# Kernel tuning notes

Hardware: AMD Instinct MI355X
Metric: run time of the kernel (lower is better)

## Reference

```python
import jax, jax.numpy as jnp
import numpy as np

# Fixed architecture constants from the source
B, T, D, V, L, H = 4096, 128, 64, 65, 3, 8
HD = D // H  # head_size = 8
DF = 4 * D   # 256


def _layernorm(x, g, b, eps=1e-5):
    mu = jnp.mean(x, axis=-1, keepdims=True)
    var = jnp.mean(jnp.square(x - mu), axis=-1, keepdims=True)
    return (x - mu) * jax.lax.rsqrt(var + eps) * g + b


def setup_inputs() -> dict:
    key = jax.random.key(0)
    ks = iter(jax.random.split(key, 64))
    s = 0.02
    n = lambda shape: jax.random.normal(next(ks), shape, dtype=jnp.float32) * s
    inp = {
        "tok_emb": n((V, D)),
        "pos_emb": n((T, D)),
        # per-block params stacked on leading layer dim L=3
        "ln1_g": jnp.ones((L, D), jnp.float32), "ln1_b": jnp.zeros((L, D), jnp.float32),
        "wq": n((L, D, D)), "wk": n((L, D, D)), "wv": n((L, D, D)),
        "wo": n((L, D, D)), "bo": jnp.zeros((L, D), jnp.float32),
        "ln2_g": jnp.ones((L, D), jnp.float32), "ln2_b": jnp.zeros((L, D), jnp.float32),
        "w1": n((L, D, DF)), "b1": jnp.zeros((L, DF), jnp.float32),
        "w2": n((L, DF, D)), "b2": jnp.zeros((L, D), jnp.float32),
        "lnf_g": jnp.ones((D,), jnp.float32), "lnf_b": jnp.zeros((D,), jnp.float32),
        "lm_w": n((D, V)), "lm_b": jnp.zeros((V,), jnp.float32),
        "idx": jax.random.randint(next(ks), (B, T), 0, V),
        "targets": jax.random.randint(next(ks), (B, T), 0, V),
    }
    return inp


def _forward(tok_emb, pos_emb, ln1_g, ln1_b, wq, wk, wv, wo, bo,
             ln2_g, ln2_b, w1, b1, w2, b2, lnf_g, lnf_b, lm_w, lm_b,
             idx, targets):
    b, t = idx.shape
    x = tok_emb[idx] + pos_emb[:t]  # [B,T,D]
    mask = jnp.tril(jnp.ones((t, t), bool))
    scale = 1.0 / np.sqrt(HD)
    for l in range(L):  # 3 structurally identical blocks (dropout = identity at eval)
        xn = _layernorm(x, ln1_g[l], ln1_b[l])
        # 8 per-head projections fused into one [D,D] matmul (concat along out dim)
        q = (xn @ wq[l]).reshape(b, t, H, HD)
        k = (xn @ wk[l]).reshape(b, t, H, HD)
        v = (xn @ wv[l]).reshape(b, t, H, HD)
        scores = jnp.einsum('bqhd,bkhd->bhqk', q, k) * scale
        scores = jnp.where(mask, scores, -jnp.inf)
        probs = jax.nn.softmax(scores, axis=-1)
        attn = jnp.einsum('bhqk,bkhd->bqhd', probs, v).reshape(b, t, D)
        x = x + attn @ wo[l] + bo[l]
        xn = _layernorm(x, ln2_g[l], ln2_b[l])
        x = x + jax.nn.relu(xn @ w1[l] + b1[l]) @ w2[l] + b2[l]
    x = _layernorm(x, lnf_g, lnf_b)
    logits = (x @ lm_w + lm_b).reshape(b * t, V)
    logp = jax.nn.log_softmax(logits, axis=-1)
    loss = -jnp.mean(jnp.take_along_axis(logp, targets.reshape(b * t, 1), axis=1))
    return logits, loss


def reference(tok_emb, pos_emb, ln1_g, ln1_b, wq, wk, wv, wo, bo,
              ln2_g, ln2_b, w1, b1, w2, b2, lnf_g, lnf_b, lm_w, lm_b,
              idx, targets):
    return _forward(tok_emb, pos_emb, ln1_g, ln1_b, wq, wk, wv, wo, bo,
                    ln2_g, ln2_b, w1, b1, w2, b2, lnf_g, lnf_b, lm_w, lm_b,
                    idx, targets)
```

## Files before the change

kernel.cpp:

```cpp
#include <hip/hip_runtime.h>
#include <hip/hip_bf16.h>

#define NB  4096
#define NT  128
#define ND  64
#define NV  65
#define NL  3
#define NH  8
#define NDF 256
#define NBT (NB*NT)

#define OFF_TOK   0
#define OFF_POS   4160
#define OFF_LN1G  12352
#define OFF_LN1B  12544
#define OFF_WQ    12736
#define OFF_WK    25024
#define OFF_WV    37312
#define OFF_WO    49600
#define OFF_BO    61888
#define OFF_LN2G  62080
#define OFF_LN2B  62272
#define OFF_W1    62464
#define OFF_B1    111616
// ... 152 lines not shown
    float var  = s2 * (1.f / 64.f) - mu * mu;
    float rstd = rsqrtf(var + 1e-5f);
    #pragma unroll
    for (int c = 0; c < 8; c++) {
        int cc = c0 + c;
        dst[r][cc] = (src[r][cc] - mu) * rstd * g[cc] + bb[cc];
    }
}

__device__ __forceinline__ void ln_frag_hi(const float (*src)[68],
        unsigned short* __restrict__ dhi,
        const float* __restrict__ g, const float* __restrict__ bb, int tid) {
    int r = tid >> 3, q = tid & 7, c0 = q * 8;
    float s = 0.f, s2 = 0.f;
    #pragma unroll
    for (int c = 0; c < 8; c++) { float v = src[r][c0 + c]; s += v; s2 += v * v; }
    s += __shfl_xor(s, 1);  s2 += __shfl_xor(s2, 1);
    s += __shfl_xor(s, 2);  s2 += __shfl_xor(s2, 2);
    s += __shfl_xor(s, 4);  s2 += __shfl_xor(s2, 4);
    float mu   = s  * (1.f / 64.f);
    float var  = s2 * (1.f / 64.f) - mu * mu;
    float rstd = rsqrtf(var + 1e-5f);
    unsigned uh[4];
    #pragma unroll
    for (int c2 = 0; c2 < 4; c2++) {
        float y0 = (src[r][c0 + c2*2    ] - mu) * rstd * g[c0 + c2*2    ] + bb[c0 + c2*2    ];
        float y1 = (src[r][c0 + c2*2 + 1] - mu) * rstd * g[c0 + c2*2 + 1] + bb[c0 + c2*2 + 1];
        uh[c2] = (unsigned)f2bf(y0) | ((unsigned)f2bf(y1) << 16);
    }
    int di = (((r >> 4) * 2 + (q >> 2)) * 64 + (q & 3) * 16 + (r & 15)) * 8;
    *(uint4*)(dhi + di) = make_uint4(uh[0], uh[1], uh[2], uh[3]);
}

__device__ __forceinline__ void fma16(const float* xr, const float* wr, float& a) {
    float4 x0 = *(const float4*)(xr);
    float4 x1 = *(const float4*)(xr + 4);
    float4 x2 = *(const float4*)(xr + 8);
    float4 x3 = *(const float4*)(xr + 12);
    a = fmaf(x0.x, wr[0],  a); a = fmaf(x0.y, wr[1],  a);
    a = fmaf(x0.z, wr[2],  a); a = fmaf(x0.w, wr[3],  a);
    a = fmaf(x1.x, wr[4],  a); a = fmaf(x1.y, wr[5],  a);
    a = fmaf(x1.z, wr[6],  a); a = fmaf(x1.w, wr[7],  a);
    a = fmaf(x2.x, wr[8],  a); a = fmaf(x2.y, wr[9],  a);
    a = fmaf(x2.z, wr[10], a); a = fmaf(x2.w, wr[11], a);
    a = fmaf(x3.x, wr[12], a); a = fmaf(x3.y, wr[13], a);
    a = fmaf(x3.z, wr[14], a); a = fmaf(x3.w, wr[15], a);
}

__device__ void ln_scalar(const float* x, float* o,
                          const float* g, const float* bb) {
    float mu = 0.f;
    for (int i = 0; i < ND; i++) mu += x[i];
    mu *= (1.f / 64.f);
    float var = 0.f;
    for (int i = 0; i < ND; i++) { float d = x[i] - mu; var += d * d; }
    var *= (1.f / 64.f);
    float rstd = rsqrtf(var + 1e-5f);
    for (int i = 0; i < ND; i++) o[i] = (x[i] - mu) * rstd * g[i] + bb[i];
}

__device__ __forceinline__ void store_o(unsigned short* xah, int mt, int head,
                                        int g, int cl, unsigned pk0, unsigned pk1) {
    if (cl < 8) {
        unsigned pk[2] = {pk0, pk1};
        #pragma unroll
        for (int i2 = 0; i2 < 4; i2++) {
            int r = mt * 16 + g * 4 + i2;
            int col = head * 8 + cl;
            unsigned v = pk[i2 >> 1];
            unsigned short hv = (unsigned short)((i2 & 1) ? (v >> 16) : (v & 0xffffu));
            int di = (((r >> 4) * 2 + (col >> 5)) * 64 + ((col >> 3) & 3) * 16
                      + (r & 15)) * 8 + (col & 7);
            xah[di] = hv;
        }
    }
}

__global__ __launch_bounds__(1024, 4) void gpt_fwd(
    const float* __restrict__ W, const unsigned short* __restrict__ pkw,
    int usepk, const void* __restrict__ idxp, const void* __restrict__ tgtp,
    float* __restrict__ out, float* __restrict__ loss_acc,
    const int* __restrict__ flags)
{
    __shared__ alignas(16) float xs[NT][68];
    __shared__ alignas(16) unsigned short xah[8192];
    __shared__ alignas(16) unsigned short uni[12288];
    __shared__ alignas(16) unsigned short zblk[8];
    __shared__ float wsum[8];

    unsigned short* q_l = uni;
    unsigned short* k_l = uni + 4096;
    unsigned short* vb  = uni + 8192;
    unsigned short* ha  = uni;

    const int tid  = threadIdx.x;
    const int lane = tid & 63;
    const int w    = tid >> 6;
    const int cl   = lane & 15;
    const int g    = lane >> 4;
    const int b    = blockIdx.x;
    const int fl   = *flags;
    if (!usepk || (fl & 8)) return;
    const bool i64 = !(fl & 4);
    const int*       idx32 = (const int*)idxp;
    const long long* idx64 = (const long long*)idxp;
    const int*       tgt32 = (const int*)tgtp;
    const long long* tgt64 = (const long long*)tgtp;

    if (tid < 8) zblk[tid] = 0;

    for (int e = tid * 4; e < NT * ND; e += 4096) {
        int r = e >> 6, c = e & 63;
        int n = b * NT + r;
        int tok = i64 ? (int)idx64[n] : idx32[n];
        float4 te = *(const float4*)&W[OFF_TOK + tok * ND + c];
        float4 pe = *(const float4*)&W[OFF_POS + r * ND + c];
        float4 xv;
        xv.x = te.x + pe.x; xv.y = te.y + pe.y;
        xv.z = te.z + pe.z; xv.w = te.w + pe.w;
        *(float4*)&xs[r][c] = xv;
    }
    __syncthreads();

    for (int lay = 0; lay < NL; lay++) {
        ln_frag_hi(xs, xah, W + OFF_LN1G + lay * 64, W + OFF_LN1B + lay * 64, tid);
        __syncthreads();

        unsigned ostash[2][2];
        const int headl = w & 3;

        #pragma unroll 1
        for (int hf = 0; hf < 2; hf++) {
            {
                const unsigned short* pbase = pkw + lay * 4096;
                #pragma unroll 1
                for (int i = 0; i < 3; i++) {
                    int ft = w * 3 + i;
                    int mat = ft >> 4;
                    int mt  = (ft >> 1) & 7;
                    int ntg = hf * 2 + (ft & 1);
                    const unsigned short* pb = pbase + mat * 12288 + ntg * 1024 + lane * 8;
                    f4v acc = {0.f, 0.f, 0.f, 0.f};
                    #pragma unroll
                    for (int kt = 0; kt < 2; kt++) {
                        s8v ah = *(const s8v*)(xah + ((mt * 2 + kt) * 64 + lane) * 8);
                        s8v bh = *(const s8v*)(pb + kt * 512);
                        s8v bl = *(const s8v*)(pb + PKLO + kt * 512);
                        acc = mfma16(ah, bh, acc);
                        acc = mfma16(ah, bl, acc);
                    }
                    int row0 = mt * 16 + g * 4;
                    int fullcol = ntg * 16 + cl;
                    int hl2 = (fullcol >> 3) & 3;
                    int dim = fullcol & 7;
                    if (mat == 0) {
                        #pragma unroll
                        for (int i2 = 0; i2 < 4; i2++)
                            q_l[(hl2 * 128 + row0 + i2) * 8 + dim] =
                                f2bf(acc[i2] * 0.35355339059327373f);
                    } else if (mat == 1) {
                        #pragma unroll
                        for (int i2 = 0; i2 < 4; i2++)
                            k_l[(hl2 * 128 + row0 + i2) * 8 + dim] = f2bf(acc[i2]);
                    } else {
                        #pragma unroll
                        for (int i2 = 0; i2 < 4; i2++) {
                            int key = row0 + i2;
                            vb[((hl2 * 4 + (key >> 5)) * 4 + ((key >> 3) & 3)) * 64
                               + dim * 8 + (key & 7)] = f2bf(acc[i2]);
                        }
                    }
                }
            }
            __syncthreads();

            {
                #pragma unroll 1
                for (int ti = 0; ti < 2; ti++) {
                    int mt = (w >> 2) + ti * 4;
                    const unsigned short* qsrc = (lane < 16)
                        ? q_l + (headl * 128 + mt * 16 + cl) * 8 : zblk;
                    s8v qb = *(const s8v*)qsrc;
                    float m = -1e30f, lsum = 0.f;
                    f4v o = {0.f, 0.f, 0.f, 0.f};
                    const int ktmax = mt >> 1;
                    #pragma unroll 1
                    for (int kt = 0; kt <= ktmax; kt++) {
                        f4v p0, p1;
                        {
                            const unsigned short* ksrc = (lane < 16)
                                ? k_l + (headl * 128 + (kt * 2) * 16 + cl) * 8 : zblk;
                            s8v kb = *(const s8v*)ksrc;
                            f4v s0 = {0.f, 0.f, 0.f, 0.f};
                            s0 = mfma16(kb, qb, s0);
                            if (kt * 2 == mt) {
                                #pragma unroll
                                for (int i2 = 0; i2 < 4; i2++)
                                    s0[i2] = (g * 4 + i2 <= cl) ? s0[i2] : -1e30f;
                            }
                            p0 = s0;
                        }
                        if (kt * 2 + 1 <= mt) {
                            const unsigned short* ksrc = (lane < 16)
                                ? k_l + (headl * 128 + (kt * 2 + 1) * 16 + cl) * 8 : zblk;
                            s8v kb = *(const s8v*)ksrc;
                            f4v s1 = {0.f, 0.f, 0.f, 0.f};
                            s1 = mfma16(kb, qb, s1);
                            if (kt * 2 + 1 == mt) {
                                #pragma unroll
                                for (int i2 = 0; i2 < 4; i2++)
                                    s1[i2] = (g * 4 + i2 <= cl) ? s1[i2] : -1e30f;
                            }
                            p1 = s1;
                        } else {
                            p1 = (f4v){-1e30f, -1e30f, -1e30f, -1e30f};
                        }
                        float bm = fmaxf(fmaxf(fmaxf(p0[0], p0[1]), fmaxf(p0[2], p0[3])),
                                         fmaxf(fmaxf(p1[0], p1[1]), fmaxf(p1[2], p1[3])));
                        bm = fmaxf(bm, __shfl_xor(bm, 16));
                        bm = fmaxf(bm, __shfl_xor(bm, 32));
                        float nm  = fmaxf(m, bm);
                        float fac = __expf(m - nm);
                        float ps = 0.f;
                        #pragma unroll
                        for (int i2 = 0; i2 < 4; i2++) {
                            p0[i2] = __expf(p0[i2] - nm); ps += p0[i2];
                            p1[i2] = __expf(p1[i2] - nm); ps += p1[i2];
                        }
                        ps += __shfl_xor(ps, 16);
                        ps += __shfl_xor(ps, 32);
                        lsum = lsum * fac + ps;
                        #pragma unroll
                        for (int i2 = 0; i2 < 4; i2++)
                            o[i2] *= __shfl(fac, g * 4 + i2);
                        float pe[8];
                        #pragma unroll
                        for (int e = 0; e < 8; e++) {
                            int src = ((g & 1) * 2 + (e >> 2)) * 16 + cl;
                            float a0 = __shfl(p0[e & 3], src);
                            float a1 = __shfl(p1[e & 3], src);
                            pe[e] = (g >> 1) ? a1 : a0;
                        }
                        union { unsigned u[4]; s8v v; } pu;
                        #pragma unroll
                        for (int j = 0; j < 4; j++)
                            pu.u[j] = (unsigned)f2bf(pe[2 * j]) |
                                      ((unsigned)f2bf(pe[2 * j + 1]) << 16);
                        s8v vf = *(const s8v*)(vb + ((headl * 4 + kt) * 4 + g) * 64
                                               + (cl & 7) * 8);
                        o = mfma16(pu.v, vf, o);
                        m = nm;
                    }
                    float inv = 1.f / lsum;
                    float invt[4];
                    #pragma unroll
                    for (int i2 = 0; i2 < 4; i2++) invt[i2] = __shfl(inv, g * 4 + i2);
                    unsigned pk0 = (unsigned)f2bf(o[0] * invt[0]) |
                                   ((unsigned)f2bf(o[1] * invt[1]) << 16);
                    unsigned pk1 = (unsigned)f2bf(o[2] * invt[2]) |
                                   ((unsigned)f2bf(o[3] * invt[3]) << 16);
                    if (hf == 0) {
                        ostash[ti][0] = pk0; ostash[ti][1] = pk1;
                    } else {
                        store_o(xah, mt, 4 + headl, g, cl, pk0, pk1);
                    }
                }
                if (hf == 1) {
                    #pragma unroll
                    for (int ti = 0; ti < 2; ti++) {
                        int mt = (w >> 2) + ti * 4;
                        store_o(xah, mt, headl, g, cl, ostash[ti][0], ostash[ti][1]);
                    }
                }
            }
            __syncthreads();
        }

        {
            const unsigned short* pbase = pkw + 36864 + lay * 4096;
            const float* bo = W + OFF_BO + lay * 64;
            #pragma unroll 1
            for (int i = 0; i < 2; i++) {
                int ft = w * 2 + i;
                int mt = ft >> 2, nt = ft & 3;
                const unsigned short* pb = pbase + nt * 1024 + lane * 8;
                f4v acc = {0.f, 0.f, 0.f, 0.f};
                #pragma unroll
                for (int kt = 0; kt < 2; kt++) {
                    s8v ah = *(const s8v*)(xah + ((mt * 2 + kt) * 64 + lane) * 8);
                    s8v bh = *(const s8v*)(pb + kt * 512);
                    s8v bl = *(const s8v*)(pb + PKLO + kt * 512);
                    acc = mfma16(ah, bh, acc);
                    acc = mfma16(ah, bl, acc);
                }
                int row0 = mt * 16 + g * 4, col = nt * 16 + cl;
                float bias = bo[col];
                #pragma unroll
                for (int i2 = 0; i2 < 4; i2++)
                    xs[row0 + i2][col] += acc[i2] + bias;
            }
        }
        __syncthreads();

        ln_frag_hi(xs, xah, W + OFF_LN2G + lay * 64, W + OFF_LN2B + lay * 64, tid);
        __syncthreads();

        #pragma unroll 1
        for (int ch = 0; ch < 4; ch++) {
            {
                const float* b1 = W + OFF_B1 + lay * 256;
                #pragma unroll 1
                for (int i = 0; i < 2; i++) {
                    int ft = w * 2 + i;
                    int mtl = ft >> 4, nt = ft & 15;
                    int mtg = ch * 2 + mtl;
                    const unsigned short* pb = pkw + 49152 + lay * 16384 + nt * 1024 + lane * 8;
                    f4v acc = {0.f, 0.f, 0.f, 0.f};
                    #pragma unroll
                    for (int kt = 0; kt < 2; kt++) {
                        s8v ah = *(const s8v*)(xah + ((mtg * 2 + kt) * 64 + lane) * 8);
                        s8v bh = *(const s8v*)(pb + kt * 512);
                        s8v bl = *(const s8v*)(pb + PKLO + kt * 512);
                        acc = mfma16(ah, bh, acc);
                        acc = mfma16(ah, bl, acc);
                    }
                    int col = nt * 16 + cl;
                    float bias = b1[col];
                    int kt2 = col >> 5, q2 = (col >> 3) & 3, e2 = col & 7;
                    #pragma unroll
                    for (int i2 = 0; i2 < 4; i2++) {
                        int lr = mtl * 16 + g * 4 + i2;
                        float hv = fmaxf(acc[i2] + bias, 0.f);
                        ha[((mtl * 8 + kt2) * 64 + q2 * 16 + (lr & 15)) * 8 + e2] = f2bf(hv);
                    }
                }
            }
            __syncthreads();
            {
                if (w < 8) {
                    const float* b2 = W + OFF_B2 + lay * 64;
                    int mtl = w >> 2, nt = w & 3;
                    const unsigned short* pb = pkw + 98304 + lay * 16384 + nt * 4096 + lane * 8;
                    f4v acc = {0.f, 0.f, 0.f, 0.f};
                    #pragma unroll 2
                    for (int kt = 0; kt < 8; kt++) {
                        s8v ah = *(const s8v*)(ha + ((mtl * 8 + kt) * 64 + lane) * 8);
                        s8v bh = *(const s8v*)(pb + kt * 512);
                        s8v bl = *(const s8v*)(pb + PKLO + kt * 512);
                        acc = mfma16(ah, bh, acc);
                        acc = mfma16(ah, bl, acc);
                    }
                    int row0 = ch * 32 + mtl * 16 + g * 4, col = nt * 16 + cl;
                    float bias = b2[col];
                    #pragma unroll
                    for (int i2 = 0; i2 < 4; i2++)
                        xs[row0 + i2][col] += acc[i2] + bias;
                }
            }
            __syncthreads();
        }
    }

    ln_frag_hi(xs, xah, W + OFF_LNFG, W + OFF_LNFB, tid);
    __syncthreads();

    if (w < 8) {
        int mt = w;
        const unsigned short* pb = pkw + 147456 + lane * 8;
        f4v acc[4];
        #pragma unroll
        for (int nt = 0; nt < 4; nt++) {
            f4v a = {0.f, 0.f, 0.f, 0.f};
            #pragma unroll
            for (int kt = 0; kt < 2; kt++) {
                s8v ah = *(const s8v*)(xah + ((mt * 2 + kt) * 64 + lane) * 8);
                s8v bh = *(const s8v*)(pb + nt * 1024 + kt * 512);
                s8v bl = *(const s8v*)(pb + PKLO + nt * 1024 + kt * 512);
                a = mfma16(ah, bh, a);
                a = mfma16(ah, bl, a);
            }
            float bias = W[OFF_LMB + nt * 16 + cl];
            #pragma unroll
            for (int i2 = 0; i2 < 4; i2++) a[i2] += bias;
            acc[nt] = a;
        }
        float l2 = 0.f;
        #pragma unroll
        for (int j = 0; j < 16; j++) {
            int d = g * 16 + j;
            int xi = ((mt * 2 + (d >> 5)) * 64 + ((d >> 3) & 3) * 16 + cl) * 8 + (d & 7);
            l2 += bf2f(xah[xi]) * W[OFF_LMW + d * 65 + 64];
        }
        l2 += __shfl_xor(l2, 16);
        l2 += __shfl_xor(l2, 32);
        l2 += W[OFF_LMB + 64];
        float l2t[4];
        #pragma unroll
        for (int i2 = 0; i2 < 4; i2++) l2t[i2] = __shfl(l2, g * 4 + i2);

        float wacc = 0.f;
        #pragma unroll
        for (int i2 = 0; i2 < 4; i2++) {
            float M = fmaxf(fmaxf(acc[0][i2], acc[1][i2]), fmaxf(acc[2][i2], acc[3][i2]));
            M = fmaxf(M, __shfl_xor(M, 1)); M = fmaxf(M, __shfl_xor(M, 2));
            M = fmaxf(M, __shfl_xor(M, 4)); M = fmaxf(M, __shfl_xor(M, 8));
            M = fmaxf(M, l2t[i2]);
            float ss = __expf(acc[0][i2] - M) + __expf(acc[1][i2] - M)
                     + __expf(acc[2][i2] - M) + __expf(acc[3][i2] - M);
            ss += __shfl_xor(ss, 1); ss += __shfl_xor(ss, 2);
            ss += __shfl_xor(ss, 4); ss += __shfl_xor(ss, 8);
            ss += __expf(l2t[i2] - M);
            float lse = M + logf(ss);
            int r = mt * 16 + g * 4 + i2;
            int row = b * NT + r;
            int tg = i64 ? (int)tgt64[row] : tgt32[row];
            float lt = 0.f;
            #pragma unroll
            for (int nt = 0; nt < 4; nt++)
                if (nt * 16 + cl == tg) lt += acc[nt][i2];
            wacc += lt;
            if (cl == 0) {
                if (tg == 64) wacc += l2t[i2];
                wacc -= lse;
                out[row * NV + 64] = l2t[i2];
            }
            #pragma unroll
            for (int nt = 0; nt < 4; nt++)
                out[row * NV + nt * 16 + cl] = acc[nt][i2];
        }
        wacc += __shfl_xor(wacc, 1);  wacc += __shfl_xor(wacc, 2);
        wacc += __shfl_xor(wacc, 4);  wacc += __shfl_xor(wacc, 8);
        wacc += __shfl_xor(wacc, 16); wacc += __shfl_xor(wacc, 32);
        if (lane == 0) wsum[w] = wacc;
    }
    __syncthreads();
    if (tid == 0) {
        float t = 0.f;
        #pragma unroll
        for (int wv = 0; wv < 8; wv++) t += wsum[wv];
        atomicAdd(loss_acc, t);
    }
    __syncthreads();

    if (b == 0 && tid == 0) {
        float x0[ND], xn0[ND], v0[ND], h0[NDF];
        int tok0 = i64 ? (int)idx64[0] : idx32[0];
        for (int c = 0; c < ND; c++)
            x0[c] = W[OFF_TOK + tok0 * ND + c] + W[OFF_POS + c];
        for (int l = 0; l < NL; l++) {
            ln_scalar(x0, xn0, W + OFF_LN1G + l * ND, W + OFF_LN1B + l * ND);
            for (int c = 0; c < ND; c++) {
                float a = 0.f;
                for (int i = 0; i < ND; i++)
                    a += xn0[i] * W[OFF_WV + l * ND * ND + i * ND + c];
                v0[c] = a;
            }
            for (int c = 0; c < ND; c++) {
                float a = W[OFF_BO + l * ND + c];
                for (int i = 0; i < ND; i++)
                    a += v0[i] * W[OFF_WO + l * ND * ND + i * ND + c];
                x0[c] += a;
            }
            ln_scalar(x0, xn0, W + OFF_LN2G + l * ND, W + OFF_LN2B + l * ND);
            for (int j = 0; j < NDF; j++) {
                float a = W[OFF_B1 + l * NDF + j];
                for (int i = 0; i < ND; i++)
                    a += xn0[i] * W[OFF_W1 + l * ND * NDF + i * NDF + j];
                h0[j] = fmaxf(a, 0.f);
            }
            for (int c = 0; c < ND; c++) {
                float a = W[OFF_B2 + l * ND + c];
                for (int j = 0; j < NDF; j++)
                    a += h0[j] * W[OFF_W2 + l * NDF * ND + j * ND + c];
                x0[c] += a;
            }
        }
        ln_scalar(x0, xn0, W + OFF_LNFG, W + OFF_LNFB);
        bool bad = false;
        for (int v = 0; v < NV; v++) {
            float lg = W[OFF_LMB + v];
            for (int i = 0; i < ND; i++)
                lg += xn0[i] * W[OFF_LMW + i * NV + v];
            if (!(fabsf(out[v] - lg) <= 0.1f)) bad = true;
        }
        if (bad) out[0] = 100.0f;
    }
}

__global__ __launch_bounds__(1024, 4) void gpt_fwd_valu(
    const float* __restrict__ W, int usepk,
    const void* __restrict__ idxp, const void* __restrict__ tgtp,
    float* __restrict__ out, float* __restrict__ loss_acc,
    const int* __restrict__ flags)
{
    const int fl = *flags;
    if (usepk && !(fl & 8)) return;

    __shared__ alignas(16) float xs[NT][68];
    __shared__ alignas(16) float xn[NT][68];
    __shared__ alignas(16) unsigned short qs[NT][72];
    __shared__ alignas(16) unsigned short ks[NT][72];
    __shared__ alignas(16) unsigned short vs[NT][72];
    __shared__ alignas(16) float hch[32][264];
    __shared__ float wsum[16];

    const int tid  = threadIdx.x;
    const int lane = tid & 63;
    const int w    = tid >> 6;
    const int b    = blockIdx.x;
    const bool i64 = !(fl & 4);
    const int*       idx32 = (const int*)idxp;
    const long long* idx64 = (const long long*)idxp;
    const int*       tgt32 = (const int*)tgtp;
    const long long* tgt64 = (const long long*)tgtp;

    for (int e = tid * 4; e < NT * ND; e += 4096) {
        int r = e >> 6, c = e & 63;
        int n = b * NT + r;
        int tok = i64 ? (int)idx64[n] : idx32[n];
        float4 te = *(const float4*)&W[OFF_TOK + tok * ND + c];
        float4 pe = *(const float4*)&W[OFF_POS + r * ND + c];
        float4 xv;
        xv.x = te.x + pe.x; xv.y = te.y + pe.y;
        xv.z = te.z + pe.z; xv.w = te.w + pe.w;
        *(float4*)&xs[r][c] = xv;
    }
    __syncthreads();
// ... 161 lines not shown
    __syncthreads();

    {
        const float* lmw = W + OFF_LMW;
        float wacc = 0.f;
        for (int rr = 0; rr < 8; rr++) {
            int r = w * 8 + rr;
            float lg  = W[OFF_LMB + lane];
            float lg2 = W[OFF_LMB + 64];
            #pragma unroll 8
            for (int i = 0; i < ND; i++) {
                float xv = xn[r][i];
                lg  = fmaf(xv, lmw[i * NV + lane], lg);
                lg2 = fmaf(xv, lmw[i * NV + 64],  lg2);
            }
            float M = lg;
            #pragma unroll
            for (int off = 32; off; off >>= 1) M = fmaxf(M, __shfl_xor(M, off));
            M = fmaxf(M, lg2);
            float ssum = __expf(lg - M);
            #pragma unroll
            for (int off = 32; off; off >>= 1) ssum += __shfl_xor(ssum, off);
            ssum += __expf(lg2 - M);
            float lse = M + logf(ssum);
            int row = b * NT + r;
            int tg  = i64 ? (int)tgt64[row] : tgt32[row];
            float lt = (tg < 64) ? __shfl(lg, tg) : lg2;
            wacc += lt - lse;
            out[row * NV + lane] = lg;
            if (lane == 0) out[row * NV + 64] = lg2;
        }
        if (lane == 0) wsum[w] = wacc;
        __syncthreads();
        if (tid == 0) {
            float t = 0.f;
            #pragma unroll
            for (int wv = 0; wv < 16; wv++) t += wsum[wv];
            atomicAdd(loss_acc, t);
        }
    }
}

__global__ void finalize_loss(const float* __restrict__ acc,
                              float* __restrict__ out) {
    out[NBT * NV] = -acc[0] * (1.f / (float)NBT);
}

extern "C" void kernel_launch(void* const* d_in, const int* in_sizes, int n_in,
                              void* d_out, int out_size, void* d_ws, size_t ws_size,
                              hipStream_t stream)
{
    static const int want[21] = {4160, 8192, 192, 192, 12288, 12288, 12288,
                                 12288, 192, 192, 192, 49152, 768, 49152, 192,
                                 64, 64, 4160, 65, 524288, 524288};
    int diag = 0;
    if (n_in != 21) diag = 3;
    else for (int i = 0; i < 21; i++) if (in_sizes[i] != want[i]) { diag = 3; break; }
    if (!diag && out_size != NBT * NV + 1) diag = 4;
    if (!diag && ws_size < (size_t)(OFF_FLAG + 1) * 4) diag = 5;
    if (diag) {
        diag_fill<<<(out_size + 255) / 256, 256, 0, stream>>>(
            (float*)d_out, out_size, (float)diag);
        return;
    }

    float* W = (float*)d_ws;
    float* loss_acc = W + OFF_LOSS;
    int*   flags    = (int*)(W + OFF_FLAG);
    hipMemsetAsync(W + OFF_LOSS, 0, 2 * sizeof(float), stream);

    detect_float<<<1, 256, 0, stream>>>((const unsigned short*)d_in[0], flags);
    detect_int  <<<1, 256, 0, stream>>>((const int*)d_in[19], flags);
    mfma_probe  <<<1, 64,  0, stream>>>(flags);

    CvtArgs a;
    for (int i = 0; i < 19; i++) a.p[i] = d_in[i];
    cvt_params<<<(CVT_TOTAL + 255) / 256, 256, 0, stream>>>(a, W, flags);

    int usepk = (ws_size >= NEED_WS) ? 1 : 0;
    unsigned short* pkw = (unsigned short*)(W + PKF);
    if (usepk)
        pack_weights<<<(PK_ELEMS + 255) / 256, 256, 0, stream>>>(W, pkw);

    gpt_fwd<<<NB, 1024, 0, stream>>>(W, pkw, usepk, d_in[19], d_in[20],
                                     (float*)d_out, loss_acc, flags);
    gpt_fwd_valu<<<NB, 1024, 0, stream>>>(W, usepk, d_in[19], d_in[20],
                                          (float*)d_out, loss_acc, flags);
    finalize_loss<<<1, 1, 0, stream>>>(loss_acc, (float*)d_out);
}
```

Measured before the change: 2.479 ms.

## Process two sequences per workgroup to reuse weight fragments across batches

Each 1024-thread workgroup now handles two batch sequences, with activation, fragment and scratch LDS buffers doubled. Weight fragments loaded from global memory are reused for both sequences' MFMAs, and the FFN2 and LM-head stages now use all 16 waves instead of 8. The grid is halved. This roughly doubles LDS per block, which may lower occupancy, and it raises register pressure because of the extra stash variables.

Measured after the change: 2.565 ms. 1.03x slower.

```diff
diff --git a/kernel.cpp b/kernel.cpp
--- a/kernel.cpp
+++ b/kernel.cpp
@@ -258,23 +258,18 @@
     float* __restrict__ out, float* __restrict__ loss_acc,
     const int* __restrict__ flags)
 {
-    __shared__ alignas(16) float xs[NT][68];
-    __shared__ alignas(16) unsigned short xah[8192];
-    __shared__ alignas(16) unsigned short uni[12288];
+    __shared__ alignas(16) float xs[2][NT][68];
+    __shared__ alignas(16) unsigned short xah[2][8192];
+    __shared__ alignas(16) unsigned short uni[2][12288];
     __shared__ alignas(16) unsigned short zblk[8];
-    __shared__ float wsum[8];
-
-    unsigned short* q_l = uni;
-    unsigned short* k_l = uni + 4096;
-    unsigned short* vb  = uni + 8192;
-    unsigned short* ha  = uni;
+    __shared__ float wsum[16];
 
     const int tid  = threadIdx.x;
     const int lane = tid & 63;
     const int w    = tid >> 6;
     const int cl   = lane & 15;
     const int g    = lane >> 4;
-    const int b    = blockIdx.x;
+    const int b0   = blockIdx.x * 2;
     const int fl   = *flags;
     if (!usepk || (fl & 8)) return;
     const bool i64 = !(fl & 4);
@@ -285,25 +280,29 @@
 
     if (tid < 8) zblk[tid] = 0;
 
-    for (int e = tid * 4; e < NT * ND; e += 4096) {
-        int r = e >> 6, c = e & 63;
-        int n = b * NT + r;
+    for (int e = tid * 4; e < 2 * NT * ND; e += 4096) {
+        int s = e >> 13;
+        int le = e & 8191;
+        int r = le >> 6, c = le & 63;
+        int n = (b0 + s) * NT + r;
         int tok = i64 ? (int)idx64[n] : idx32[n];
         float4 te = *(const float4*)&W[OFF_TOK + tok * ND + c];
         float4 pe = *(const float4*)&W[OFF_POS + r * ND + c];
         float4 xv;
         xv.x = te.x + pe.x; xv.y = te.y + pe.y;
         xv.z = te.z + pe.z; xv.w = te.w + pe.w;
-        *(float4*)&xs[r][c] = xv;
+        *(float4*)&xs[s][r][c] = xv;
     }
     __syncthreads();
 
     for (int lay = 0; lay < NL; lay++) {
-        ln_frag_hi(xs, xah, W + OFF_LN1G + lay * 64, W + OFF_LN1B + lay * 64, tid);
+        ln_frag_hi(xs[0], xah[0], W + OFF_LN1G + lay * 64, W + OFF_LN1B + lay * 64, tid);
+        ln_frag_hi(xs[1], xah[1], W + OFF_LN1G + lay * 64, W + OFF_LN1B + lay * 64, tid);
         __syncthreads();
 
-        unsigned ostash[2][2];
         const int headl = w & 3;
+        unsigned st0a = 0, st0b = 0, st1a = 0, st1b = 0;
+        unsigned st2a = 0, st2b = 0, st3a = 0, st3b = 0;
 
         #pragma unroll 1
         for (int hf = 0; hf < 2; hf++) {
@@ -316,34 +315,42 @@
                     int mt  = (ft >> 1) & 7;
                     int ntg = hf * 2 + (ft & 1);
                     const unsigned short* pb = pbase + mat * 12288 + ntg * 1024 + lane * 8;
-                    f4v acc = {0.f, 0.f, 0.f, 0.f};
-                    #pragma unroll
-                    for (int kt = 0; kt < 2; kt++) {
-                        s8v ah = *(const s8v*)(xah + ((mt * 2 + kt) * 64 + lane) * 8);
-                        s8v bh = *(const s8v*)(pb + kt * 512);
-                        s8v bl = *(const s8v*)(pb + PKLO + kt * 512);
-                        acc = mfma16(ah, bh, acc);
-                        acc = mfma16(ah, bl, acc);
-                    }
+                    s8v bh0 = *(const s8v*)(pb);
+                    s8v bl0 = *(const s8v*)(pb + PKLO);
+                    s8v bh1 = *(const s8v*)(pb + 512);
+                    s8v bl1 = *(const s8v*)(pb + PKLO + 512);
                     int row0 = mt * 16 + g * 4;
                     int fullcol = ntg * 16 + cl;
                     int hl2 = (fullcol >> 3) & 3;
                     int dim = fullcol & 7;
-                    if (mat == 0) {
-                        #pragma unroll
-                        for (int i2 = 0; i2 < 4; i2++)
-                            q_l[(hl2 * 128 + row0 + i2) * 8 + dim] =
-                                f2bf(acc[i2] * 0.35355339059327373f);
-                    } else if (mat == 1) {
-                        #pragma unroll
-                        for (int i2 = 0; i2 < 4; i2++)
-                            k_l[(hl2 * 128 + row0 + i2) * 8 + dim] = f2bf(acc[i2]);
-                    } else {
-                        #pragma unroll
-                        for (int i2 = 0; i2 < 4; i2++) {
-                            int key = row0 + i2;
-                            vb[((hl2 * 4 + (key >> 5)) * 4 + ((key >> 3) & 3)) * 64
-                               + dim * 8 + (key & 7)] = f2bf(acc[i2]);
+                    #pragma unroll
+                    for (int s = 0; s < 2; s++) {
+                        s8v a0 = *(const s8v*)(xah[s] + ((mt * 2    ) * 64 + lane) * 8);
+                        s8v a1 = *(const s8v*)(xah[s] + ((mt * 2 + 1) * 64 + lane) * 8);
+                        f4v acc = {0.f, 0.f, 0.f, 0.f};
+                        acc = mfma16(a0, bh0, acc);
+                        acc = mfma16(a0, bl0, acc);
+                        acc = mfma16(a1, bh1, acc);
+                        acc = mfma16(a1, bl1, acc);
+                        unsigned short* q_l = uni[s];
+                        unsigned short* k_l = uni[s] + 4096;
+                        unsigned short* vb  = uni[s] + 8192;
+                        if (mat == 0) {
+                            #pragma unroll
+                            for (int i2 = 0; i2 < 4; i2++)
+                                q_l[(hl2 * 128 + row0 + i2) * 8 + dim] =
+                                    f2bf(acc[i2] * 0.35355339059327373f);
+                        } else if (mat == 1) {
+                            #pragma unroll
+                            for (int i2 = 0; i2 < 4; i2++)
+                                k_l[(hl2 * 128 + row0 + i2) * 8 + dim] = f2bf(acc[i2]);
+                        } else {
+                            #pragma unroll
+                            for (int i2 = 0; i2 < 4; i2++) {
+                                int key = row0 + i2;
+                                vb[((hl2 * 4 + (key >> 5)) * 4 + ((key >> 3) & 3)) * 64
+                                   + dim * 8 + (key & 7)] = f2bf(acc[i2]);
+                            }
                         }
                     }
                 }
@@ -352,7 +359,11 @@
 
             {
                 #pragma unroll 1
-                for (int ti = 0; ti < 2; ti++) {
+                for (int sti = 0; sti < 4; sti++) {
+                    int s = sti & 1, ti = sti >> 1;
+                    unsigned short* q_l = uni[s];
+                    unsigned short* k_l = uni[s] + 4096;
+                    unsigned short* vb  = uni[s] + 8192;
                     int mt = (w >> 2) + ti * 4;
                     const unsigned short* qsrc = (lane < 16)
                         ? q_l + (headl * 128 + mt * 16 + cl) * 8 : zblk;
@@ -436,17 +447,22 @@
                     unsigned pk1 = (unsigned)f2bf(o[2] * invt[2]) |
                                    ((unsigned)f2bf(o[3] * invt[3]) << 16);
                     if (hf == 0) {
-                        ostash[ti][0] = pk0; ostash[ti][1] = pk1;
+                        switch (sti) {
+                            case 0:  st0a = pk0; st0b = pk1; break;
+                            case 1:  st1a = pk0; st1b = pk1; break;
+                            case 2:  st2a = pk0; st2b = pk1; break;
+                            default: st3a = pk0; st3b = pk1; break;
+                        }
                     } else {
-                        store_o(xah, mt, 4 + headl, g, cl, pk0, pk1);
+                        store_o(xah[s], mt, 4 + headl, g, cl, pk0, pk1);
                     }
                 }
                 if (hf == 1) {
-                    #pragma unroll
-                    for (int ti = 0; ti < 2; ti++) {
-                        int mt = (w >> 2) + ti * 4;
-                        store_o(xah, mt, headl, g, cl, ostash[ti][0], ostash[ti][1]);
-                    }
+                    int mt0 = (w >> 2), mt1 = (w >> 2) + 4;
+                    store_o(xah[0], mt0, headl, g, cl, st0a, st0b);
+                    store_o(xah[1], mt0, headl, g, cl, st1a, st1b);
+                    store_o(xah[0], mt1, headl, g, cl, st2a, st2b);
+                    store_o(xah[1], mt1, headl, g, cl, st3a, st3b);
                 }
             }
             __syncthreads();
@@ -460,88 +476,101 @@
                 int ft = w * 2 + i;
                 int mt = ft >> 2, nt = ft & 3;
                 const unsigned short* pb = pbase + nt * 1024 + lane * 8;
-                f4v acc = {0.f, 0.f, 0.f, 0.f};
-                #pragma unroll
-                for (int kt = 0; kt < 2; kt++) {
-                    s8v ah = *(const s8v*)(xah + ((mt * 2 + kt) * 64 + lane) * 8);
-                    s8v bh = *(const s8v*)(pb + kt * 512);
-                    s8v bl = *(const s8v*)(pb + PKLO + kt * 512);
-                    acc = mfma16(ah, bh, acc);
-                    acc = mfma16(ah, bl, acc);
-                }
+                s8v bh0 = *(const s8v*)(pb);
+                s8v bl0 = *(const s8v*)(pb + PKLO);
+                s8v bh1 = *(const s8v*)(pb + 512);
+                s8v bl1 = *(const s8v*)(pb + PKLO + 512);
                 int row0 = mt * 16 + g * 4, col = nt * 16 + cl;
                 float bias = bo[col];
                 #pragma unroll
-                for (int i2 = 0; i2 < 4; i2++)
-                    xs[row0 + i2][col] += acc[i2] + bias;
+                for (int s = 0; s < 2; s++) {
+                    s8v a0 = *(const s8v*)(xah[s] + ((mt * 2    ) * 64 + lane) * 8);
+                    s8v a1 = *(const s8v*)(xah[s] + ((mt * 2 + 1) * 64 + lane) * 8);
+                    f4v acc = {0.f, 0.f, 0.f, 0.f};
+                    acc = mfma16(a0, bh0, acc);
+                    acc = mfma16(a0, bl0, acc);
+                    acc = mfma16(a1, bh1, acc);
+                    acc = mfma16(a1, bl1, acc);
+                    #pragma unroll
+                    for (int i2 = 0; i2 < 4; i2++)
+                        xs[s][row0 + i2][col] += acc[i2] + bias;
+                }
             }
         }
         __syncthreads();
 
-        ln_frag_hi(xs, xah, W + OFF_LN2G + lay * 64, W + OFF_LN2B + lay * 64, tid);
+        ln_frag_hi(xs[0], xah[0], W + OFF_LN2G + lay * 64, W + OFF_LN2B + lay * 64, tid);
+        ln_frag_hi(xs[1], xah[1], W + OFF_LN2G + lay * 64, W + OFF_LN2B + lay * 64, tid);
         __syncthreads();
 
         #pragma unroll 1
         for (int ch = 0; ch < 4; ch++) {
             {
-                const float* b1 = W + OFF_B1 + lay * 256;
+                const float* b1p = W + OFF_B1 + lay * 256;
                 #pragma unroll 1
                 for (int i = 0; i < 2; i++) {
                     int ft = w * 2 + i;
                     int mtl = ft >> 4, nt = ft & 15;
                     int mtg = ch * 2 + mtl;
                     const unsigned short* pb = pkw + 49152 + lay * 16384 + nt * 1024 + lane * 8;
-                    f4v acc = {0.f, 0.f, 0.f, 0.f};
-                    #pragma unroll
-                    for (int kt = 0; kt < 2; kt++) {
-                        s8v ah = *(const s8v*)(xah + ((mtg * 2 + kt) * 64 + lane) * 8);
-                        s8v bh = *(const s8v*)(pb + kt * 512);
-                        s8v bl = *(const s8v*)(pb + PKLO + kt * 512);
-                        acc = mfma16(ah, bh, acc);
-                        acc = mfma16(ah, bl, acc);
-                    }
+                    s8v bh0 = *(const s8v*)(pb);
+                    s8v bl0 = *(const s8v*)(pb + PKLO);
+                    s8v bh1 = *(const s8v*)(pb + 512);
+                    s8v bl1 = *(const s8v*)(pb + PKLO + 512);
                     int col = nt * 16 + cl;
-                    float bias = b1[col];
+                    float bias = b1p[col];
                     int kt2 = col >> 5, q2 = (col >> 3) & 3, e2 = col & 7;
                     #pragma unroll
-                    for (int i2 = 0; i2 < 4; i2++) {
-                        int lr = mtl * 16 + g * 4 + i2;
-                        float hv = fmaxf(acc[i2] + bias, 0.f);
-                        ha[((mtl * 8 + kt2) * 64 + q2 * 16 + (lr & 15)) * 8 + e2] = f2bf(hv);
+                    for (int s = 0; s < 2; s++) {
+                        s8v a0 = *(const s8v*)(xah[s] + ((mtg * 2    ) * 64 + lane) * 8);
+                        s8v a1 = *(const s8v*)(xah[s] + ((mtg * 2 + 1) * 64 + lane) * 8);
+                        f4v acc = {0.f, 0.f, 0.f, 0.f};
+                        acc = mfma16(a0, bh0, acc);
+                        acc = mfma16(a0, bl0, acc);
+                        acc = mfma16(a1, bh1, acc);
+                        acc = mfma16(a1, bl1, acc);
+                        unsigned short* ha = uni[s];
+                        #pragma unroll
+                        for (int i2 = 0; i2 < 4; i2++) {
+                            int lr = mtl * 16 + g * 4 + i2;
+                            float hv = fmaxf(acc[i2] + bias, 0.f);
+                            ha[((mtl * 8 + kt2) * 64 + q2 * 16 + (lr & 15)) * 8 + e2] = f2bf(hv);
+                        }
                     }
                 }
             }
             __syncthreads();
             {
-                if (w < 8) {
-                    const float* b2 = W + OFF_B2 + lay * 64;
-                    int mtl = w >> 2, nt = w & 3;
-                    const unsigned short* pb = pkw + 98304 + lay * 16384 + nt * 4096 + lane * 8;
-                    f4v acc = {0.f, 0.f, 0.f, 0.f};
-                    #pragma unroll 2
-                    for (int kt = 0; kt < 8; kt++) {
-                        s8v ah = *(const s8v*)(ha + ((mtl * 8 + kt) * 64 + lane) * 8);
-                        s8v bh = *(const s8v*)(pb + kt * 512);
-                        s8v bl = *(const s8v*)(pb + PKLO + kt * 512);
-                        acc = mfma16(ah, bh, acc);
-                        acc = mfma16(ah, bl, acc);
-                    }
-                    int row0 = ch * 32 + mtl * 16 + g * 4, col = nt * 16 + cl;
-                    float bias = b2[col];
-                    #pragma unroll
-                    for (int i2 = 0; i2 < 4; i2++)
-                        xs[row0 + i2][col] += acc[i2] + bias;
-                }
+                const float* b2p = W + OFF_B2 + lay * 64;
+                int s = w >> 3, t8 = w & 7;
+                int mtl = t8 >> 2, nt = t8 & 3;
+                const unsigned short* pb = pkw + 98304 + lay * 16384 + nt * 4096 + lane * 8;
+                unsigned short* ha = uni[s];
+                f4v acc = {0.f, 0.f, 0.f, 0.f};
+                #pragma unroll 2
+                for (int kt = 0; kt < 8; kt++) {
+                    s8v ah = *(const s8v*)(ha + ((mtl * 8 + kt) * 64 + lane) * 8);
+                    s8v bh = *(const s8v*)(pb + kt * 512);
+                    s8v bl = *(const s8v*)(pb + PKLO + kt * 512);
+                    acc = mfma16(ah, bh, acc);
+                    acc = mfma16(ah, bl, acc);
+                }
+                int row0 = ch * 32 + mtl * 16 + g * 4, col = nt * 16 + cl;
+                float bias = b2p[col];
+                #pragma unroll
+                for (int i2 = 0; i2 < 4; i2++)
+                    xs[s][row0 + i2][col] += acc[i2] + bias;
             }
             __syncthreads();
         }
     }
 
-    ln_frag_hi(xs, xah, W + OFF_LNFG, W + OFF_LNFB, tid);
+    ln_frag_hi(xs[0], xah[0], W + OFF_LNFG, W + OFF_LNFB, tid);
+    ln_frag_hi(xs[1], xah[1], W + OFF_LNFG, W + OFF_LNFB, tid);
     __syncthreads();
 
-    if (w < 8) {
-        int mt = w;
+    {
+        int s = w >> 3, mt = w & 7;
         const unsigned short* pb = pkw + 147456 + lane * 8;
         f4v acc[4];
         #pragma unroll
@@ -549,7 +578,7 @@
             f4v a = {0.f, 0.f, 0.f, 0.f};
             #pragma unroll
             for (int kt = 0; kt < 2; kt++) {
-                s8v ah = *(const s8v*)(xah + ((mt * 2 + kt) * 64 + lane) * 8);
+                s8v ah = *(const s8v*)(xah[s] + ((mt * 2 + kt) * 64 + lane) * 8);
                 s8v bh = *(const s8v*)(pb + nt * 1024 + kt * 512);
                 s8v bl = *(const s8v*)(pb + PKLO + nt * 1024 + kt * 512);
                 a = mfma16(ah, bh, a);
@@ -565,7 +594,7 @@
         for (int j = 0; j < 16; j++) {
             int d = g * 16 + j;
             int xi = ((mt * 2 + (d >> 5)) * 64 + ((d >> 3) & 3) * 16 + cl) * 8 + (d & 7);
-            l2 += bf2f(xah[xi]) * W[OFF_LMW + d * 65 + 64];
+            l2 += bf2f(xah[s][xi]) * W[OFF_LMW + d * 65 + 64];
         }
         l2 += __shfl_xor(l2, 16);
         l2 += __shfl_xor(l2, 32);
@@ -588,7 +617,7 @@
             ss += __expf(l2t[i2] - M);
             float lse = M + logf(ss);
             int r = mt * 16 + g * 4 + i2;
-            int row = b * NT + r;
+            int row = (b0 + s) * NT + r;
             int tg = i64 ? (int)tgt64[row] : tgt32[row];
             float lt = 0.f;
             #pragma unroll
@@ -613,12 +642,12 @@
     if (tid == 0) {
         float t = 0.f;
         #pragma unroll
-        for (int wv = 0; wv < 8; wv++) t += wsum[wv];
+        for (int wv = 0; wv < 16; wv++) t += wsum[wv];
         atomicAdd(loss_acc, t);
     }
     __syncthreads();
 
-    if (b == 0 && tid == 0) {
+    if (b0 == 0 && tid == 0) {
         float x0[ND], xn0[ND], v0[ND], h0[NDF];
         int tok0 = i64 ? (int)idx64[0] : idx32[0];
         for (int c = 0; c < ND; c++)
@@ -946,8 +975,8 @@
     if (usepk)
         pack_weights<<<(PK_ELEMS + 255) / 256, 256, 0, stream>>>(W, pkw);
 
-    gpt_fwd<<<NB, 1024, 0, stream>>>(W, pkw, usepk, d_in[19], d_in[20],
-                                     (float*)d_out, loss_acc, flags);
+    gpt_fwd<<<NB / 2, 1024, 0, stream>>>(W, pkw, usepk, d_in[19], d_in[20],
+                                         (float*)d_out, loss_acc, flags);
     gpt_fwd_valu<<<NB, 1024, 0, stream>>>(W, usepk, d_in[19], d_in[20],
                                           (float*)d_out, loss_acc, flags);
     finalize_loss<<<1, 1, 0, stream>>>(loss_acc, (float*)d_out);
```

## Enlarge shared buffers to process all heads and full MLP in one pass

Applied to the files above, without the earlier changes.

Grows the shared scratch buffer from 24KB to 64KB so Q/K/V for all 8 heads and the full 128x256 hidden MLP activation fit at once. The QKV projection and attention become a single pass over all heads, and the MLP runs as one up-projection phase and one down-projection phase instead of four row chunks. This removes several block-wide barriers and idle waves (the w<8 branch in the down projection), and it makes the ostash register staging unnecessary. The cost is much higher LDS use per block, which may cut occupancy (launch bounds request 4 blocks of 1024 threads).

New measurement: 2.473 ms. Within noise of the previous version (-0.3%).

```diff
diff --git a/kernel.cpp b/kernel.cpp
--- a/kernel.cpp
+++ b/kernel.cpp
@@ -260,13 +260,13 @@
 {
     __shared__ alignas(16) float xs[NT][68];
     __shared__ alignas(16) unsigned short xah[8192];
-    __shared__ alignas(16) unsigned short uni[12288];
+    __shared__ alignas(16) unsigned short uni[32768];
     __shared__ alignas(16) unsigned short zblk[8];
     __shared__ float wsum[8];
 
     unsigned short* q_l = uni;
-    unsigned short* k_l = uni + 4096;
-    unsigned short* vb  = uni + 8192;
+    unsigned short* k_l = uni + 8192;
+    unsigned short* vb  = uni + 16384;
     unsigned short* ha  = uni;
 
     const int tid  = threadIdx.x;
@@ -302,155 +302,140 @@
         ln_frag_hi(xs, xah, W + OFF_LN1G + lay * 64, W + OFF_LN1B + lay * 64, tid);
         __syncthreads();
 
-        unsigned ostash[2][2];
-        const int headl = w & 3;
-
-        #pragma unroll 1
-        for (int hf = 0; hf < 2; hf++) {
-            {
-                const unsigned short* pbase = pkw + lay * 4096;
+        {
+            const unsigned short* pbase = pkw + lay * 4096;
+            #pragma unroll 1
+            for (int i = 0; i < 6; i++) {
+                int ft = w * 6 + i;
+                int mat = ft >> 5;
+                int rem = ft & 31;
+                int mt  = rem >> 2;
+                int ntg = rem & 3;
+                const unsigned short* pb = pbase + mat * 12288 + ntg * 1024 + lane * 8;
+                f4v acc = {0.f, 0.f, 0.f, 0.f};
+                #pragma unroll
+                for (int kt = 0; kt < 2; kt++) {
+                    s8v ah = *(const s8v*)(xah + ((mt * 2 + kt) * 64 + lane) * 8);
+                    s8v bh = *(const s8v*)(pb + kt * 512);
+                    s8v bl = *(const s8v*)(pb + PKLO + kt * 512);
+                    acc = mfma16(ah, bh, acc);
+                    acc = mfma16(ah, bl, acc);
+                }
+                int row0 = mt * 16 + g * 4;
+                int fullcol = ntg * 16 + cl;
+                int head = fullcol >> 3;
+                int dim  = fullcol & 7;
+                if (mat == 0) {
+                    #pragma unroll
+                    for (int i2 = 0; i2 < 4; i2++)
+                        q_l[(head * 128 + row0 + i2) * 8 + dim] =
+                            f2bf(acc[i2] * 0.35355339059327373f);
+                } else if (mat == 1) {
+                    #pragma unroll
+                    for (int i2 = 0; i2 < 4; i2++)
+                        k_l[(head * 128 + row0 + i2) * 8 + dim] = f2bf(acc[i2]);
+                } else {
+                    #pragma unroll
+                    for (int i2 = 0; i2 < 4; i2++) {
+                        int key = row0 + i2;
+                        vb[((head * 4 + (key >> 5)) * 4 + ((key >> 3) & 3)) * 64
+                           + dim * 8 + (key & 7)] = f2bf(acc[i2]);
+                    }
+                }
+            }
+        }
+        __syncthreads();
+
+        {
+            #pragma unroll 1
+            for (int ti = 0; ti < 4; ti++) {
+                int t = w + ti * 16;
+                int head = t & 7, mt = t >> 3;
+                const unsigned short* qsrc = (lane < 16)
+                    ? q_l + (head * 128 + mt * 16 + cl) * 8 : zblk;
+                s8v qb = *(const s8v*)qsrc;
+                float m = -1e30f, lsum = 0.f;
+                f4v o = {0.f, 0.f, 0.f, 0.f};
+                const int ktmax = mt >> 1;
                 #pragma unroll 1
-                for (int i = 0; i < 3; i++) {
-                    int ft = w * 3 + i;
-                    int mat = ft >> 4;
-                    int mt  = (ft >> 1) & 7;
-                    int ntg = hf * 2 + (ft & 1);
-                    const unsigned short* pb = pbase + mat * 12288 + ntg * 1024 + lane * 8;
-                    f4v acc = {0.f, 0.f, 0.f, 0.f};
-                    #pragma unroll
-                    for (int kt = 0; kt < 2; kt++) {
-                        s8v ah = *(const s8v*)(xah + ((mt * 2 + kt) * 64 + lane) * 8);
-                        s8v bh = *(const s8v*)(pb + kt * 512);
-                        s8v bl = *(const s8v*)(pb + PKLO + kt * 512);
-                        acc = mfma16(ah, bh, acc);
-                        acc = mfma16(ah, bl, acc);
+                for (int kt = 0; kt <= ktmax; kt++) {
+                    f4v p0, p1;
+                    {
+                        const unsigned short* ksrc = (lane < 16)
+                            ? k_l + (head * 128 + (kt * 2) * 16 + cl) * 8 : zblk;
+                        s8v kb = *(const s8v*)ksrc;
+                        f4v s0 = {0.f, 0.f, 0.f, 0.f};
+                        s0 = mfma16(kb, qb, s0);
+                        if (kt * 2 == mt) {
+                            #pragma unroll
+                            for (int i2 = 0; i2 < 4; i2++)
+                                s0[i2] = (g * 4 + i2 <= cl) ? s0[i2] : -1e30f;
+                        }
+                        p0 = s0;
                     }
-                    int row0 = mt * 16 + g * 4;
-                    int fullcol = ntg * 16 + cl;
-                    int hl2 = (fullcol >> 3) & 3;
-                    int dim = fullcol & 7;
-                    if (mat == 0) {
-                        #pragma unroll
-                        for (int i2 = 0; i2 < 4; i2++)
-                            q_l[(hl2 * 128 + row0 + i2) * 8 + dim] =
-                                f2bf(acc[i2] * 0.35355339059327373f);
-                    } else if (mat == 1) {
-                        #pragma unroll
-                        for (int i2 = 0; i2 < 4; i2++)
-                            k_l[(hl2 * 128 + row0 + i2) * 8 + dim] = f2bf(acc[i2]);
+                    if (kt * 2 + 1 <= mt) {
+                        const unsigned short* ksrc = (lane < 16)
+                            ? k_l + (head * 128 + (kt * 2 + 1) * 16 + cl) * 8 : zblk;
+                        s8v kb = *(const s8v*)ksrc;
+                        f4v s1 = {0.f, 0.f, 0.f, 0.f};
+                        s1 = mfma16(kb, qb, s1);
+                        if (kt * 2 + 1 == mt) {
+                            #pragma unroll
+                            for (int i2 = 0; i2 < 4; i2++)
+                                s1[i2] = (g * 4 + i2 <= cl) ? s1[i2] : -1e30f;
+                        }
+                        p1 = s1;
                     } else {
-                        #pragma unroll
-                        for (int i2 = 0; i2 < 4; i2++) {
-                            int key = row0 + i2;
-                            vb[((hl2 * 4 + (key >> 5)) * 4 + ((key >> 3) & 3)) * 64
-                               + dim * 8 + (key & 7)] = f2bf(acc[i2]);
-                        }
+                        p1 = (f4v){-1e30f, -1e30f, -1e30f, -1e30f};
                     }
-                }
-            }
-            __syncthreads();
-
-            {
-                #pragma unroll 1
-                for (int ti = 0; ti < 2; ti++) {
-                    int mt = (w >> 2) + ti * 4;
-                    const unsigned short* qsrc = (lane < 16)
-                        ? q_l + (headl * 128 + mt * 16 + cl) * 8 : zblk;
-                    s8v qb = *(const s8v*)qsrc;
-                    float m = -1e30f, lsum = 0.f;
-                    f4v o = {0.f, 0.f, 0.f, 0.f};
-                    const int ktmax = mt >> 1;
-                    #pragma unroll 1
-                    for (int kt = 0; kt <= ktmax; kt++) {
-                        f4v p0, p1;
-                        {
-                            const unsigned short* ksrc = (lane < 16)
-                                ? k_l + (headl * 128 + (kt * 2) * 16 + cl) * 8 : zblk;
-                            s8v kb = *(const s8v*)ksrc;
-                            f4v s0 = {0.f, 0.f, 0.f, 0.f};
-                            s0 = mfma16(kb, qb, s0);
-                            if (kt * 2 == mt) {
-                                #pragma unroll
-                                for (int i2 = 0; i2 < 4; i2++)
-                                    s0[i2] = (g * 4 + i2 <= cl) ? s0[i2] : -1e30f;
-                            }
-                            p0 = s0;
-                        }
-                        if (kt * 2 + 1 <= mt) {
-                            const unsigned short* ksrc = (lane < 16)
-                                ? k_l + (headl * 128 + (kt * 2 + 1) * 16 + cl) * 8 : zblk;
-                            s8v kb = *(const s8v*)ksrc;
-                            f4v s1 = {0.f, 0.f, 0.f, 0.f};
-                            s1 = mfma16(kb, qb, s1);
-                            if (kt * 2 + 1 == mt) {
-                                #pragma unroll
-                                for (int i2 = 0; i2 < 4; i2++)
-                                    s1[i2] = (g * 4 + i2 <= cl) ? s1[i2] : -1e30f;
-                            }
-                            p1 = s1;
-                        } else {
-                            p1 = (f4v){-1e30f, -1e30f, -1e30f, -1e30f};
-                        }
-                        float bm = fmaxf(fmaxf(fmaxf(p0[0], p0[1]), fmaxf(p0[2], p0[3])),
-                                         fmaxf(fmaxf(p1[0], p1[1]), fmaxf(p1[2], p1[3])));
-                        bm = fmaxf(bm, __shfl_xor(bm, 16));
-                        bm = fmaxf(bm, __shfl_xor(bm, 32));
-                        float nm  = fmaxf(m, bm);
-                        float fac = __expf(m - nm);
-                        float ps = 0.f;
-                        #pragma unroll
-                        for (int i2 = 0; i2 < 4; i2++) {
-                            p0[i2] = __expf(p0[i2] - nm); ps += p0[i2];
-                            p1[i2] = __expf(p1[i2] - nm); ps += p1[i2];
-                        }
-                        ps += __shfl_xor(ps, 16);
-                        ps += __shfl_xor(ps, 32);
-                        lsum = lsum * fac + ps;
-                        #pragma unroll
-                        for (int i2 = 0; i2 < 4; i2++)
-                            o[i2] *= __shfl(fac, g * 4 + i2);
-                        float pe[8];
-                        #pragma unroll
-                        for (int e = 0; e < 8; e++) {
-                            int src = ((g & 1) * 2 + (e >> 2)) * 16 + cl;
-                            float a0 = __shfl(p0[e & 3], src);
-                            float a1 = __shfl(p1[e & 3], src);
-                            pe[e] = (g >> 1) ? a1 : a0;
-                        }
-                        union { unsigned u[4]; s8v v; } pu;
-                        #pragma unroll
-                        for (int j = 0; j < 4; j++)
-                            pu.u[j] = (unsigned)f2bf(pe[2 * j]) |
-                                      ((unsigned)f2bf(pe[2 * j + 1]) << 16);
-                        s8v vf = *(const s8v*)(vb + ((headl * 4 + kt) * 4 + g) * 64
-                                               + (cl & 7) * 8);
-                        o = mfma16(pu.v, vf, o);
-                        m = nm;
+                    float bm = fmaxf(fmaxf(fmaxf(p0[0], p0[1]), fmaxf(p0[2], p0[3])),
+                                     fmaxf(fmaxf(p1[0], p1[1]), fmaxf(p1[2], p1[3])));
+                    bm = fmaxf(bm, __shfl_xor(bm, 16));
+                    bm = fmaxf(bm, __shfl_xor(bm, 32));
+                    float nm  = fmaxf(m, bm);
+                    float fac = __expf(m - nm);
+                    float ps = 0.f;
+                    #pragma unroll
+                    for (int i2 = 0; i2 < 4; i2++) {
+                        p0[i2] = __expf(p0[i2] - nm); ps += p0[i2];
+                        p1[i2] = __expf(p1[i2] - nm); ps += p1[i2];
                     }
-                    float inv = 1.f / lsum;
-                    float invt[4];
-                    #pragma unroll
-                    for (int i2 = 0; i2 < 4; i2++) invt[i2] = __shfl(inv, g * 4 + i2);
-                    unsigned pk0 = (unsigned)f2bf(o[0] * invt[0]) |
-                                   ((unsigned)f2bf(o[1] * invt[1]) << 16);
-                    unsigned pk1 = (unsigned)f2bf(o[2] * invt[2]) |
-                                   ((unsigned)f2bf(o[3] * invt[3]) << 16);
-                    if (hf == 0) {
-                        ostash[ti][0] = pk0; ostash[ti][1] = pk1;
-                    } else {
-                        store_o(xah, mt, 4 + headl, g, cl, pk0, pk1);
+                    ps += __shfl_xor(ps, 16);
+                    ps += __shfl_xor(ps, 32);
+                    lsum = lsum * fac + ps;
+                    #pragma unroll
+                    for (int i2 = 0; i2 < 4; i2++)
+                        o[i2] *= __shfl(fac, g * 4 + i2);
+                    float pe[8];
+                    #pragma unroll
+                    for (int e = 0; e < 8; e++) {
+                        int src = ((g & 1) * 2 + (e >> 2)) * 16 + cl;
+                        float a0 = __shfl(p0[e & 3], src);
+                        float a1 = __shfl(p1[e & 3], src);
+                        pe[e] = (g >> 1) ? a1 : a0;
                     }
-                }
-                if (hf == 1) {
-                    #pragma unroll
-                    for (int ti = 0; ti < 2; ti++) {
-                        int mt = (w >> 2) + ti * 4;
-                        store_o(xah, mt, headl, g, cl, ostash[ti][0], ostash[ti][1]);
-                    }
-                }
-            }
-            __syncthreads();
-        }
+                    union { unsigned u[4]; s8v v; } pu;
+                    #pragma unroll
+                    for (int j = 0; j < 4; j++)
+                        pu.u[j] = (unsigned)f2bf(pe[2 * j]) |
+                                  ((unsigned)f2bf(pe[2 * j + 1]) << 16);
+                    s8v vf = *(const s8v*)(vb + ((head * 4 + kt) * 4 + g) * 64
+                                           + (cl & 7) * 8);
+                    o = mfma16(pu.v, vf, o);
+                    m = nm;
+                }
+                float inv = 1.f / lsum;
+                float invt[4];
+                #pragma unroll
+                for (int i2 = 0; i2 < 4; i2++) invt[i2] = __shfl(inv, g * 4 + i2);
+                unsigned pk0 = (unsigned)f2bf(o[0] * invt[0]) |
+                               ((unsigned)f2bf(o[1] * invt[1]) << 16);
+                unsigned pk1 = (unsigned)f2bf(o[2] * invt[2]) |
+                               ((unsigned)f2bf(o[3] * invt[3]) << 16);
+                store_o(xah, mt, head, g, cl, pk0, pk1);
+            }
+        }
+        __syncthreads();
 
         {
             const unsigned short* pbase = pkw + 36864 + lay * 4096;
@@ -481,60 +466,59 @@
         ln_frag_hi(xs, xah, W + OFF_LN2G + lay * 64, W + OFF_LN2B + lay * 64, tid);
         __syncthreads();
 
-        #pragma unroll 1
-        for (int ch = 0; ch < 4; ch++) {
-            {
-                const float* b1 = W + OFF_B1 + lay * 256;
-                #pragma unroll 1
-                for (int i = 0; i < 2; i++) {
-                    int ft = w * 2 + i;
-                    int mtl = ft >> 4, nt = ft & 15;
-                    int mtg = ch * 2 + mtl;
-                    const unsigned short* pb = pkw + 49152 + lay * 16384 + nt * 1024 + lane * 8;
-                    f4v acc = {0.f, 0.f, 0.f, 0.f};
-                    #pragma unroll
-                    for (int kt = 0; kt < 2; kt++) {
-                        s8v ah = *(const s8v*)(xah + ((mtg * 2 + kt) * 64 + lane) * 8);
-                        s8v bh = *(const s8v*)(pb + kt * 512);
-                        s8v bl = *(const s8v*)(pb + PKLO + kt * 512);
-                        acc = mfma16(ah, bh, acc);
-                        acc = mfma16(ah, bl, acc);
-                    }
-                    int col = nt * 16 + cl;
-                    float bias = b1[col];
-                    int kt2 = col >> 5, q2 = (col >> 3) & 3, e2 = col & 7;
-                    #pragma unroll
-                    for (int i2 = 0; i2 < 4; i2++) {
-                        int lr = mtl * 16 + g * 4 + i2;
-                        float hv = fmaxf(acc[i2] + bias, 0.f);
-                        ha[((mtl * 8 + kt2) * 64 + q2 * 16 + (lr & 15)) * 8 + e2] = f2bf(hv);
-                    }
-                }
-            }
-            __syncthreads();
-            {
-                if (w < 8) {
-                    const float* b2 = W + OFF_B2 + lay * 64;
-                    int mtl = w >> 2, nt = w & 3;
-                    const unsigned short* pb = pkw + 98304 + lay * 16384 + nt * 4096 + lane * 8;
-                    f4v acc = {0.f, 0.f, 0.f, 0.f};
-                    #pragma unroll 2
-                    for (int kt = 0; kt < 8; kt++) {
-                        s8v ah = *(const s8v*)(ha + ((mtl * 8 + kt) * 64 + lane) * 8);
-                        s8v bh = *(const s8v*)(pb + kt * 512);
-                        s8v bl = *(const s8v*)(pb + PKLO + kt * 512);
-                        acc = mfma16(ah, bh, acc);
-                        acc = mfma16(ah, bl, acc);
-                    }
-                    int row0 = ch * 32 + mtl * 16 + g * 4, col = nt * 16 + cl;
-                    float bias = b2[col];
-                    #pragma unroll
-                    for (int i2 = 0; i2 < 4; i2++)
-                        xs[row0 + i2][col] += acc[i2] + bias;
-                }
-            }
-            __syncthreads();
-        }
+        {
+            const float* b1 = W + OFF_B1 + lay * 256;
+            #pragma unroll 1
+            for (int i = 0; i < 8; i++) {
+                int ft = w * 8 + i;
+                int mtg = ft >> 4, nt = ft & 15;
+                const unsigned short* pb = pkw + 49152 + lay * 16384 + nt * 1024 + lane * 8;
+                f4v acc = {0.f, 0.f, 0.f, 0.f};
+                #pragma unroll
+                for (int kt = 0; kt < 2; kt++) {
+                    s8v ah = *(const s8v*)(xah + ((mtg * 2 + kt) * 64 + lane) * 8);
+                    s8v bh = *(const s8v*)(pb + kt * 512);
+                    s8v bl = *(const s8v*)(pb + PKLO + kt * 512);
+                    acc = mfma16(ah, bh, acc);
+                    acc = mfma16(ah, bl, acc);
+                }
+                int col = nt * 16 + cl;
+                float bias = b1[col];
+                int kt2 = col >> 5, q2 = (col >> 3) & 3, e2 = col & 7;
+                #pragma unroll
+                for (int i2 = 0; i2 < 4; i2++) {
+                    int lr = g * 4 + i2;
+                    float hv = fmaxf(acc[i2] + bias, 0.f);
+                    ha[((mtg * 8 + kt2) * 64 + q2 * 16 + lr) * 8 + e2] = f2bf(hv);
+                }
+            }
+        }
+        __syncthreads();
+
+        {
+            const float* b2 = W + OFF_B2 + lay * 64;
+            #pragma unroll 1
+            for (int i = 0; i < 2; i++) {
+                int ft = w * 2 + i;
+                int mtl = ft >> 2, nt = ft & 3;
+                const unsigned short* pb = pkw + 98304 + lay * 16384 + nt * 4096 + lane * 8;
+                f4v acc = {0.f, 0.f, 0.f, 0.f};
+                #pragma unroll 2
+                for (int kt = 0; kt < 8; kt++) {
+                    s8v ah = *(const s8v*)(ha + ((mtl * 8 + kt) * 64 + lane) * 8);
+                    s8v bh = *(const s8v*)(pb + kt * 512);
+                    s8v bl = *(const s8v*)(pb + PKLO + kt * 512);
+                    acc = mfma16(ah, bh, acc);
+                    acc = mfma16(ah, bl, acc);
+                }
+                int row0 = mtl * 16 + g * 4, col = nt * 16 + cl;
+                float bias = b2[col];
+                #pragma unroll
+                for (int i2 = 0; i2 < 4; i2++)
+                    xs[row0 + i2][col] += acc[i2] + bias;
+            }
+        }
+        __syncthreads();
     }
 
     ln_frag_hi(xs, xah, W + OFF_LNFG, W + OFF_LNFB, tid);
```
